# Performance work log

Hardware: AMD Instinct MI355X
Metric: run time of the kernel (lower is better)

## Reference

```python
import jax, jax.numpy as jnp
import numpy as np

DIM = 2048
HIDDEN = 2048
HEADS = 4
HD = HIDDEN // HEADS  # head_dim = 512
EPS = 1e-6
BATCH = 4
SEQ = 2048


def setup_inputs() -> dict:
    key = jax.random.key(0)
    k0, k1, k2, k3 = jax.random.split(key, 4)
    s = 0.02  # typical init scale; keeps exp() input gate well-behaved
    x = jax.random.normal(k0, (BATCH, SEQ, DIM), dtype=jnp.float32)
    W_in = (jax.random.normal(k1, (HIDDEN, DIM), dtype=jnp.float32) * s)
    W_gate = (jax.random.normal(k2, (4 * HIDDEN, HIDDEN), dtype=jnp.float32) * s)
    b_gate = jnp.zeros((4 * HIDDEN,), dtype=jnp.float32)
    rms_w = jnp.ones((HD,), dtype=jnp.float32)
    W_out = (jax.random.normal(k3, (DIM, HIDDEN), dtype=jnp.float32) * s)
    return {"x": x, "W_in": W_in, "W_gate": W_gate, "b_gate": b_gate,
            "rms_w": rms_w, "W_out": W_out}


def reference(x, W_in, W_gate, b_gate, rms_w, W_out):
    B, L, _ = x.shape
    # in_proj then gate_proj (the rearrange round-trip in torch is an identity
    # on the flat hidden dim, so gates come straight from x @ W_in.T)
    xp = x @ W_in.T                                    # (B, L, HIDDEN)
    gates = xp @ W_gate.T + b_gate                     # (B, L, 4*HIDDEN)
    # rearrange 'b l (h d) -> b h l d' with h=HEADS, d=4*HD
    gates = gates.reshape(B, L, HEADS, 4 * HD).transpose(0, 2, 1, 3)
    i_g, f_g, o_g, c_t = jnp.split(gates, 4, axis=-1)  # each (B, H, L, HD)
    i_g = jnp.exp(i_g)            # exponential input gate
    f_g = jax.nn.sigmoid(f_g)
    o_g = jax.nn.sigmoid(o_g)
    c_t = jnp.tanh(c_t)

    # time-major for the recurrent scan: (L, B, H, HD)
    tm = lambda a: jnp.moveaxis(a, 2, 0)

    def step(c, g):
        i, f, o, cd = g
        c = f * c + i * cd                                         # cell update
        c_norm = c * jax.lax.rsqrt(jnp.mean(c * c, axis=-1, keepdims=True) + EPS) * rms_w
        h = o * jnp.tanh(c_norm)
        return c, h

    c0 = jnp.zeros((B, HEADS, HD), dtype=x.dtype)
    _, hs = jax.lax.scan(step, c0, (tm(i_g), tm(f_g), tm(o_g), tm(c_t)))
    # (L, B, H, HD) -> (B, L, H*HD)
    h_out = jnp.moveaxis(hs, 0, 1).reshape(B, L, HIDDEN)
    return h_out @ W_out.T                             # (B, L, DIM)
```

## Files before the change

kernel.cpp:

```cpp
#include <hip/hip_runtime.h>
#include <hip/hip_bf16.h>
#include <stdint.h>

#define DIMN    2048
#define HIDDEN  2048
#define NHEADS  4
#define HDIM    512
#define BATCH   4
#define SEQ     2048
#define NTOK    (BATCH*SEQ)
#define G4      (4*HIDDEN)
#define EPSV    1e-6f
#define CHUNK   128
#define NCHUNK  (SEQ/CHUNK)

typedef short short8 __attribute__((ext_vector_type(8)));
typedef float floatx4 __attribute__((ext_vector_type(4)));

union BV8 { uint4 u; __hip_bfloat16 h[8]; unsigned short s[8]; };

__device__ __forceinline__ float fast_sigmoid(float x) {
    return 1.0f / (1.0f + __expf(-x));
}
__device__ __forceinline__ float fast_tanh(float x) {
    return 1.0f - 2.0f / (__expf(2.0f * x) + 1.0f);
}
__device__ __forceinline__ float b2f(unsigned short u) {
    union { unsigned int ui; float f; } v; v.ui = ((unsigned int)u) << 16; return v.f;
}

__device__ __forceinline__ void gld_lds16(const void* gp, void* lp) {
    __builtin_amdgcn_global_load_lds(
        (const __attribute__((address_space(1))) void*)gp,
        (__attribute__((address_space(3))) void*)lp, 16, 0, 0);
}

__global__ __launch_bounds__(256) void cast_f32_bf16(
    const float* __restrict__ in, __hip_bfloat16* __restrict__ out, int n8)
{
    int i = blockIdx.x * 256 + threadIdx.x;
    if (i >= n8) return;
    const float4* p = (const float4*)(in + (size_t)i * 8);
    float4 a = p[0], b = p[1];
    BV8 v;
    v.h[0] = __float2bfloat16(a.x); v.h[1] = __float2bfloat16(a.y);
    v.h[2] = __float2bfloat16(a.z); v.h[3] = __float2bfloat16(a.w);
    v.h[4] = __float2bfloat16(b.x); v.h[5] = __float2bfloat16(b.y);
    v.h[6] = __float2bfloat16(b.z); v.h[7] = __float2bfloat16(b.w);
    *(uint4*)(out + (size_t)i * 8) = v.u;
}

template <int EPILOGUE, int ASRC>
__global__ __launch_bounds__(512, 2) void gemm256(
    const __hip_bfloat16* __restrict__ A,
    const __hip_bfloat16* __restrict__ Bt,
    void* __restrict__ Cout,
    const float* __restrict__ bias,
    int M, int N, int K, int lda)
{
    __shared__ __align__(16) short sA[2][256 * 64];
    __shared__ __align__(16) short sB[2][256 * 64];

    const int tid  = threadIdx.x;
    const int wave = tid >> 6, lane = tid & 63;
    const int wm = wave >> 2, wn = wave & 3;
    const int quad = lane >> 4, lr = lane & 15;
    const int r8  = lane >> 3;
    const int gcs = ((lane & 7) ^ r8) * 8;
    const int rl7 = lr & 7;

    const int gx   = gridDim.x;
    const int nwg  = gx * gridDim.y;
    const int orig = blockIdx.y * gx + blockIdx.x;
    const int wg   = (orig & 7) * (nwg >> 3) + (orig >> 3);
    const int bm = wg / gx, bn = wg % gx;

    const short* Ag = (const short*)A + (size_t)(bm * 256) * lda;
    const short* Bg = (const short*)Bt + (size_t)(bn * 256) * K;

    floatx4 acc[8][4];
#pragma unroll
    for (int i = 0; i < 8; ++i)
#pragma unroll
        for (int j = 0; j < 4; ++j) acc[i][j] = (floatx4)0.0f;

    const int NT = K >> 6;

    auto stageA = [&](int kt, int qm) {
        const int kb = kt << 6;
        size_t acol;
        if (ASRC == 0) acol = (size_t)(kb + gcs);
        else           acol = (size_t)(((kb >> 9) << 11) + (kb & 511) + gcs);
        short* dst = &sA[kt & 1][0];
#pragma unroll
        for (int e = 0; e < 2; ++e) {
            const int base = qm * 128 + e * 64 + wave * 8;
            const int row  = base + r8;
            const int grow = ((row >> 6) & 1) * 128 + qm * 64 + (row & 63);
            gld_lds16(Ag + (size_t)grow * lda + acol, dst + base * 64);
        }
    };
    auto stageB = [&](int kt, int qn) {
        const int kb = kt << 6;
        short* dst = &sB[kt & 1][0];
#pragma unroll
        for (int e = 0; e < 2; ++e) {
            const int base = qn * 128 + e * 64 + wave * 8;
            const int row  = base + r8;
            const int grow = ((row >> 5) & 3) * 64 + qn * 32 + (row & 31);
            gld_lds16(Bg + (size_t)grow * K + kb + gcs, dst + base * 64);
        }
    };

    stageA(0, 0); stageB(0, 0); stageB(0, 1); stageA(0, 1);
    stageA(1, 0); stageB(1, 0); stageB(1, 1);
    asm volatile("s_waitcnt vmcnt(6)" ::: "memory");
    __builtin_amdgcn_s_barrier();

    short8 av[4][2], b0[2][2], b1[2][2];

    for (int t = 0; t < NT; ++t) {
        const short* lA = &sA[t & 1][0];
        const short* lB = &sB[t & 1][0];

#pragma unroll
        for (int kc = 0; kc < 2; ++kc) {
            const int co = (((kc * 4 + quad) ^ rl7) << 3);
#pragma unroll
            for (int m = 0; m < 4; ++m)
                av[m][kc] = *(const short8*)&lA[(wm * 64 + m * 16 + lr) * 64 + co];
#pragma unroll
            for (int j = 0; j < 2; ++j)
                b0[j][kc] = *(const short8*)&lB[(wn * 32 + j * 16 + lr) * 64 + co];
        }
        if (t + 1 < NT) stageA(t + 1, 1);
        __builtin_amdgcn_s_setprio(1);
#pragma unroll
        for (int m = 0; m < 4; ++m)
#pragma unroll
            for (int j = 0; j < 2; ++j)
#pragma unroll
                for (int kc = 0; kc < 2; ++kc)
                    acc[m][j] = __builtin_amdgcn_mfma_f32_16x16x32_bf16(
                        av[m][kc], b0[j][kc], acc[m][j], 0, 0, 0);
        __builtin_amdgcn_s_setprio(0);
        __builtin_amdgcn_s_barrier();

#pragma unroll
        for (int kc = 0; kc < 2; ++kc) {
            const int co = (((kc * 4 + quad) ^ rl7) << 3);
#pragma unroll
            for (int j = 0; j < 2; ++j)
                b1[j][kc] = *(const short8*)&lB[(128 + wn * 32 + j * 16 + lr) * 64 + co];
        }
        if (t + 2 < NT) stageA(t + 2, 0);
        __builtin_amdgcn_s_setprio(1);
#pragma unroll
        for (int m = 0; m < 4; ++m)
#pragma unroll
            for (int j = 0; j < 2; ++j)
#pragma unroll
                for (int kc = 0; kc < 2; ++kc)
                    acc[m][2 + j] = __builtin_amdgcn_mfma_f32_16x16x32_bf16(
                        av[m][kc], b1[j][kc], acc[m][2 + j], 0, 0, 0);
        __builtin_amdgcn_s_setprio(0);
        __builtin_amdgcn_s_barrier();

#pragma unroll
        for (int kc = 0; kc < 2; ++kc) {
            const int co = (((kc * 4 + quad) ^ rl7) << 3);
#pragma unroll
            for (int m = 0; m < 4; ++m)
                av[m][kc] = *(const short8*)&lA[(128 + wm * 64 + m * 16 + lr) * 64 + co];
        }
        if (t + 2 < NT) stageB(t + 2, 0);
        __builtin_amdgcn_s_setprio(1);
#pragma unroll
        for (int m = 0; m < 4; ++m)
#pragma unroll
            for (int j = 0; j < 2; ++j)
#pragma unroll
                for (int kc = 0; kc < 2; ++kc)
                    acc[4 + m][2 + j] = __builtin_amdgcn_mfma_f32_16x16x32_bf16(
                        av[m][kc], b1[j][kc], acc[4 + m][2 + j], 0, 0, 0);
        __builtin_amdgcn_s_setprio(0);
        __builtin_amdgcn_s_barrier();

        if (t + 2 < NT) stageB(t + 2, 1);
        __builtin_amdgcn_s_setprio(1);
#pragma unroll
        for (int m = 0; m < 4; ++m)
#pragma unroll
            for (int j = 0; j < 2; ++j)
#pragma unroll
                for (int kc = 0; kc < 2; ++kc)
                    acc[4 + m][j] = __builtin_amdgcn_mfma_f32_16x16x32_bf16(
                        av[m][kc], b0[j][kc], acc[4 + m][j], 0, 0, 0);
        __builtin_amdgcn_s_setprio(0);
        if (t < NT - 2)       asm volatile("s_waitcnt vmcnt(6)" ::: "memory");
        else if (t == NT - 2) asm volatile("s_waitcnt vmcnt(0)" ::: "memory");
        __builtin_amdgcn_s_barrier();
    }

    const int colbase = bn * 256 + wn * 64;
    const int rowbase = bm * 256 + wm * 128;

    if (EPILOGUE == 0) {
        __hip_bfloat16* O = (__hip_bfloat16*)Cout;
#pragma unroll
        for (int mt = 0; mt < 8; ++mt)
#pragma unroll
            for (int nt = 0; nt < 4; ++nt)
#pragma unroll
                for (int r = 0; r < 4; ++r) {
                    int row = rowbase + mt * 16 + quad * 4 + r;
                    int col = colbase + nt * 16 + lr;
                    O[(size_t)row * N + col] = __float2bfloat16(acc[mt][nt][r]);
                }
    } else if (EPILOGUE == 1) {
        __hip_bfloat16* O = (__hip_bfloat16*)Cout;
#pragma unroll
        for (int nt = 0; nt < 4; ++nt) {
            int col = colbase + nt * 16 + lr;
            int g = (col >> 9) & 3;
            float bv = bias[col];
#pragma unroll
            for (int mt = 0; mt < 8; ++mt)
#pragma unroll
                for (int r = 0; r < 4; ++r) {
                    int row = rowbase + mt * 16 + quad * 4 + r;
                    float v = acc[mt][nt][r] + bv;
                    if (g == 0)       v = __expf(v);
                    else if (g == 3)  v = fast_tanh(v);
                    else              v = fast_sigmoid(v);
                    O[(size_t)row * N + col] = __float2bfloat16(v);
                }
        }
    } else {
        float* O = (float*)Cout;
#pragma unroll
        for (int mt = 0; mt < 8; ++mt)
#pragma unroll
            for (int nt = 0; nt < 4; ++nt)
#pragma unroll
                for (int r = 0; r < 4; ++r) {
                    int row = rowbase + mt * 16 + quad * 4 + r;
                    int col = colbase + nt * 16 + lr;
                    O[(size_t)row * N + col] = acc[mt][nt][r];
                }
    }
}

struct G16 { unsigned short i[16], f[16], c[16]; };

__device__ __forceinline__ void load_g16(const unsigned short* __restrict__ g,
                                         int t0, G16& o)
{
#pragma unroll
    for (int j = 0; j < 16; ++j) {
        const unsigned short* gp = g + (size_t)(t0 + j) * G4;
        o.i[j] = gp[0]; o.f[j] = gp[512]; o.c[j] = gp[1536];
    }
}
__device__ __forceinline__ void comp_sum16(const G16& gg, float& c, float& P)
{
#pragma unroll
    for (int j = 0; j < 16; ++j) {
        float iv = b2f(gg.i[j]);
        float fv = b2f(gg.f[j]);
        float cd = b2f(gg.c[j]);
        c = fmaf(fv, c, iv * cd);
        P *= fv;
    }
}
__device__ __forceinline__ float comp_lds16(const G16& gg, float c,
                                            __hip_bfloat16* __restrict__ sc,
                                            int t0, int d)
{
#pragma unroll
    for (int j = 0; j < 16; ++j) {
        float iv = b2f(gg.i[j]);
        float fv = b2f(gg.f[j]);
        float cd = b2f(gg.c[j]);
        c = fmaf(fv, c, iv * cd);
        sc[(t0 + j) * HDIM + d] = __float2bfloat16(c);
    }
    return c;
}

__global__ __launch_bounds__(256) void scan_pass1(
    const __hip_bfloat16* __restrict__ gates,
    float* __restrict__ cLast, float* __restrict__ PLast)
{
    int blk = blockIdx.x;
    int dh = blk & 1;
    int j  = (blk >> 1) & 15;
    int bh = blk >> 5;
    int b = bh >> 2, h = bh & 3;
    int d = dh * 256 + threadIdx.x;
    int bhd = bh * 512 + d;

    const unsigned short* g = (const unsigned short*)gates
        + (size_t)(b * SEQ + j * CHUNK) * G4 + h * 2048 + d;

    float c = 0.0f, P = 1.0f;
    G16 A, B;
    load_g16(g, 0, A);
    for (int t0 = 0; t0 < CHUNK; t0 += 32) {
        load_g16(g, t0 + 16, B);
        comp_sum16(A, c, P);
        if (t0 + 32 < CHUNK) load_g16(g, t0 + 32, A);
        comp_sum16(B, c, P);
    }
    cLast[j * 8192 + bhd] = c;
    PLast[j * 8192 + bhd] = P;
}

__global__ __launch_bounds__(512) void scan_pass2_norm(
    const __hip_bfloat16* __restrict__ gates_c,
    const float* __restrict__ cLast, const float* __restrict__ PLast,
    __hip_bfloat16* __restrict__ gates,
    const float* __restrict__ rms_w)
{
    __shared__ __hip_bfloat16 sc[CHUNK * HDIM];

    int blk = blockIdx.x;
    int j  = blk & 15;
    int bh = blk >> 4;
    int b = bh >> 2, h = bh & 3;
    int d = threadIdx.x;
    int bhd = bh * 512 + d;

    float c = 0.0f;
    for (int k = 0; k < j; ++k)
        c = fmaf(PLast[k * 8192 + bhd], c, cLast[k * 8192 + bhd]);

    const unsigned short* g = (const unsigned short*)gates_c
        + (size_t)(b * SEQ + j * CHUNK) * G4 + h * 2048 + d;

    G16 A, B;
    load_g16(g, 0, A);
    for (int t0 = 0; t0 < CHUNK; t0 += 32) {
        load_g16(g, t0 + 16, B);
        c = comp_lds16(A, c, sc, t0, d);
        if (t0 + 32 < CHUNK) load_g16(g, t0 + 32, A);
        c = comp_lds16(B, c, sc, t0 + 16, d);
    }
    __syncthreads();

    const int wave = threadIdx.x >> 6, lane = threadIdx.x & 63;

    float4 w0 = *(const float4*)&rms_w[lane * 8];
    float4 w1 = *(const float4*)&rms_w[lane * 8 + 4];
    float w[8] = { w0.x, w0.y, w0.z, w0.w, w1.x, w1.y, w1.z, w1.w };

    for (int it = 0; it < 16; ++it) {
        int t = wave * 16 + it;
        size_t tok = (size_t)(b * SEQ + j * CHUNK + t);

        BV8 cv; cv.u = *(const uint4*)&sc[t * HDIM + lane * 8];
        float cf[8]; float s = 0.0f;
#pragma unroll
        for (int q = 0; q < 8; ++q) { cf[q] = b2f(cv.s[q]); s += cf[q] * cf[q]; }
#pragma unroll
        for (int off = 32; off > 0; off >>= 1) s += __shfl_xor(s, off, 64);
        float rs = rsqrtf(s * (1.0f / 512.0f) + EPSV);

        BV8 ov; ov.u = *(const uint4*)(gates + tok * G4 + h * 2048 + 1024 + lane * 8);
        BV8 hv;
#pragma unroll
        for (int q = 0; q < 8; ++q) {
            float o = b2f(ov.s[q]);
            hv.h[q] = __float2bfloat16(o * fast_tanh(cf[q] * rs * w[q]));
        }
        *(uint4*)(gates + tok * G4 + h * 2048 + lane * 8) = hv.u;
    }
}

extern "C" void kernel_launch(void* const* d_in, const int* in_sizes, int n_in,
                              void* d_out, int out_size, void* d_ws, size_t ws_size,
                              hipStream_t stream)
{
    const float* x      = (const float*)d_in[0];
    const float* W_in   = (const float*)d_in[1];
    const float* W_gate = (const float*)d_in[2];
    const float* b_gate = (const float*)d_in[3];
    const float* rms_w  = (const float*)d_in[4];
    const float* W_out  = (const float*)d_in[5];
    float* out = (float*)d_out;

    char* base = (char*)d_ws;
    __hip_bfloat16* wgb   = (__hip_bfloat16*)base;
    __hip_bfloat16* xpb   = (__hip_bfloat16*)(base + (((size_t)32) << 20));
    __hip_bfloat16* gates = (__hip_bfloat16*)(base + (((size_t)64) << 20));
    __hip_bfloat16* wib  = gates;
    __hip_bfloat16* xb   = (__hip_bfloat16*)(base + (((size_t)72) << 20));
    __hip_bfloat16* wob  = wgb;
    float* cLast = (float*)(base + (((size_t)8) << 20));
    float* PLast = (float*)(base + (((size_t)8) << 20) + (512 << 10));

    cast_f32_bf16<<<(HIDDEN * DIMN) / 8 / 256, 256, 0, stream>>>(W_in, wib, (HIDDEN * DIMN) / 8);
    cast_f32_bf16<<<(NTOK * DIMN) / 8 / 256, 256, 0, stream>>>(x, xb, (NTOK * DIMN) / 8);
    cast_f32_bf16<<<(G4 * HIDDEN) / 8 / 256, 256, 0, stream>>>(W_gate, wgb, (G4 * HIDDEN) / 8);

    {
        dim3 grid(HIDDEN / 256, NTOK / 256);
        gemm256<0, 0><<<grid, 512, 0, stream>>>(xb, wib, xpb, nullptr,
                                                NTOK, HIDDEN, DIMN, DIMN);
    }
    {
        dim3 grid(G4 / 256, NTOK / 256);
        gemm256<1, 0><<<grid, 512, 0, stream>>>(xpb, wgb, gates, b_gate,
                                                NTOK, G4, HIDDEN, HIDDEN);
    }
    cast_f32_bf16<<<(DIMN * HIDDEN) / 8 / 256, 256, 0, stream>>>(W_out, wob, (DIMN * HIDDEN) / 8);

    scan_pass1<<<BATCH * NHEADS * NCHUNK * 2, 256, 0, stream>>>(gates, cLast, PLast);
    scan_pass2_norm<<<BATCH * NHEADS * NCHUNK, 512, 0, stream>>>(gates, cLast, PLast,
                                                                 gates, rms_w);

    {
        dim3 grid(DIMN / 256, NTOK / 256);
        gemm256<2, 1><<<grid, 512, 0, stream>>>(gates, wob, out, nullptr,
                                                NTOK, DIMN, HIDDEN, G4);
    }
}
```

Baseline: 636.7 us.

## Rework GEMM to 4 waves with 128x128 per-wave tiles and simpler pipeline

The 256x256 GEMM moves from 8 waves (each computing 128x64) to 4 waves (each computing 128x128 with 64 accumulators), which raises register reuse of the A and B fragments. The staggered quarter-tile staging with partial vmcnt waits and s_setprio is replaced by one combined A+B stage per k-step, a full vmcnt(0) wait and a single barrier. This cuts LDS read traffic per MFMA and barrier count, but needs much higher register pressure (256 accumulator VGPRs), allows at most one block per CU, and loads the next tile less overlapped with compute.

```diff
diff --git a/kernel.cpp b/kernel.cpp
--- a/kernel.cpp
+++ b/kernel.cpp
@@ -51,7 +51,7 @@
 }
 
 template <int EPILOGUE, int ASRC>
-__global__ __launch_bounds__(512, 2) void gemm256(
+__global__ __launch_bounds__(256, 1) void gemm256(
     const __hip_bfloat16* __restrict__ A,
     const __hip_bfloat16* __restrict__ Bt,
     void* __restrict__ Cout,
@@ -63,7 +63,7 @@
 
     const int tid  = threadIdx.x;
     const int wave = tid >> 6, lane = tid & 63;
-    const int wm = wave >> 2, wn = wave & 3;
+    const int wm = wave >> 1, wn = wave & 1;
     const int quad = lane >> 4, lr = lane & 15;
     const int r8  = lane >> 3;
     const int gcs = ((lane & 7) ^ r8) * 8;
@@ -78,131 +78,78 @@
     const short* Ag = (const short*)A + (size_t)(bm * 256) * lda;
     const short* Bg = (const short*)Bt + (size_t)(bn * 256) * K;
 
-    floatx4 acc[8][4];
+    floatx4 acc[8][8];
 #pragma unroll
     for (int i = 0; i < 8; ++i)
 #pragma unroll
-        for (int j = 0; j < 4; ++j) acc[i][j] = (floatx4)0.0f;
+        for (int j = 0; j < 8; ++j) acc[i][j] = (floatx4)0.0f;
 
     const int NT = K >> 6;
 
-    auto stageA = [&](int kt, int qm) {
+    auto stageAB = [&](int kt) {
         const int kb = kt << 6;
         size_t acol;
         if (ASRC == 0) acol = (size_t)(kb + gcs);
         else           acol = (size_t)(((kb >> 9) << 11) + (kb & 511) + gcs);
-        short* dst = &sA[kt & 1][0];
-#pragma unroll
-        for (int e = 0; e < 2; ++e) {
-            const int base = qm * 128 + e * 64 + wave * 8;
-            const int row  = base + r8;
-            const int grow = ((row >> 6) & 1) * 128 + qm * 64 + (row & 63);
-            gld_lds16(Ag + (size_t)grow * lda + acol, dst + base * 64);
+        short* dA = &sA[kt & 1][0];
+        short* dB = &sB[kt & 1][0];
+#pragma unroll
+        for (int c = 0; c < 8; ++c) {
+            const int base = c * 32 + wave * 8;
+            const int grow = base + r8;
+            gld_lds16(Ag + (size_t)grow * lda + acol,   dA + base * 64);
+            gld_lds16(Bg + (size_t)grow * K + kb + gcs, dB + base * 64);
         }
     };
-    auto stageB = [&](int kt, int qn) {
-        const int kb = kt << 6;
-        short* dst = &sB[kt & 1][0];
-#pragma unroll
-        for (int e = 0; e < 2; ++e) {
-            const int base = qn * 128 + e * 64 + wave * 8;
-            const int row  = base + r8;
-            const int grow = ((row >> 5) & 3) * 64 + qn * 32 + (row & 31);
-            gld_lds16(Bg + (size_t)grow * K + kb + gcs, dst + base * 64);
-        }
-    };
-
-    stageA(0, 0); stageB(0, 0); stageB(0, 1); stageA(0, 1);
-    stageA(1, 0); stageB(1, 0); stageB(1, 1);
-    asm volatile("s_waitcnt vmcnt(6)" ::: "memory");
+
+    stageAB(0);
+    asm volatile("s_waitcnt vmcnt(0)" ::: "memory");
     __builtin_amdgcn_s_barrier();
 
-    short8 av[4][2], b0[2][2], b1[2][2];
+    short8 av[8], bv[8];
 
     for (int t = 0; t < NT; ++t) {
         const short* lA = &sA[t & 1][0];
         const short* lB = &sB[t & 1][0];
 
-#pragma unroll
-        for (int kc = 0; kc < 2; ++kc) {
-            const int co = (((kc * 4 + quad) ^ rl7) << 3);
-#pragma unroll
-            for (int m = 0; m < 4; ++m)
-                av[m][kc] = *(const short8*)&lA[(wm * 64 + m * 16 + lr) * 64 + co];
-#pragma unroll
-            for (int j = 0; j < 2; ++j)
-                b0[j][kc] = *(const short8*)&lB[(wn * 32 + j * 16 + lr) * 64 + co];
-        }
-        if (t + 1 < NT) stageA(t + 1, 1);
-        __builtin_amdgcn_s_setprio(1);
-#pragma unroll
-        for (int m = 0; m < 4; ++m)
-#pragma unroll
-            for (int j = 0; j < 2; ++j)
-#pragma unroll
-                for (int kc = 0; kc < 2; ++kc)
-                    acc[m][j] = __builtin_amdgcn_mfma_f32_16x16x32_bf16(
-                        av[m][kc], b0[j][kc], acc[m][j], 0, 0, 0);
-        __builtin_amdgcn_s_setprio(0);
+        {
+            const int co = ((quad ^ rl7) << 3);
+#pragma unroll
+            for (int mt = 0; mt < 8; ++mt)
+                av[mt] = *(const short8*)&lA[(wm * 128 + mt * 16 + lr) * 64 + co];
+#pragma unroll
+            for (int nt = 0; nt < 8; ++nt)
+                bv[nt] = *(const short8*)&lB[(wn * 128 + nt * 16 + lr) * 64 + co];
+        }
+        if (t + 1 < NT) stageAB(t + 1);
+#pragma unroll
+        for (int mt = 0; mt < 8; ++mt)
+#pragma unroll
+            for (int nt = 0; nt < 8; ++nt)
+                acc[mt][nt] = __builtin_amdgcn_mfma_f32_16x16x32_bf16(
+                    av[mt], bv[nt], acc[mt][nt], 0, 0, 0);
+
+        {
+            const int co = (((4 + quad) ^ rl7) << 3);
+#pragma unroll
+            for (int mt = 0; mt < 8; ++mt)
+                av[mt] = *(const short8*)&lA[(wm * 128 + mt * 16 + lr) * 64 + co];
+#pragma unroll
+            for (int nt = 0; nt < 8; ++nt)
+                bv[nt] = *(const short8*)&lB[(wn * 128 + nt * 16 + lr) * 64 + co];
+        }
+#pragma unroll
+        for (int mt = 0; mt < 8; ++mt)
+#pragma unroll
+            for (int nt = 0; nt < 8; ++nt)
+                acc[mt][nt] = __builtin_amdgcn_mfma_f32_16x16x32_bf16(
+                    av[mt], bv[nt], acc[mt][nt], 0, 0, 0);
+
+        if (t + 1 < NT) asm volatile("s_waitcnt vmcnt(0)" ::: "memory");
         __builtin_amdgcn_s_barrier();
-
-#pragma unroll
-        for (int kc = 0; kc < 2; ++kc) {
-            const int co = (((kc * 4 + quad) ^ rl7) << 3);
-#pragma unroll
-            for (int j = 0; j < 2; ++j)
-                b1[j][kc] = *(const short8*)&lB[(128 + wn * 32 + j * 16 + lr) * 64 + co];
-        }
-        if (t + 2 < NT) stageA(t + 2, 0);
-        __builtin_amdgcn_s_setprio(1);
-#pragma unroll
-        for (int m = 0; m < 4; ++m)
-#pragma unroll
-            for (int j = 0; j < 2; ++j)
-#pragma unroll
-                for (int kc = 0; kc < 2; ++kc)
-                    acc[m][2 + j] = __builtin_amdgcn_mfma_f32_16x16x32_bf16(
-                        av[m][kc], b1[j][kc], acc[m][2 + j], 0, 0, 0);
-        __builtin_amdgcn_s_setprio(0);
-        __builtin_amdgcn_s_barrier();
-
-#pragma unroll
-        for (int kc = 0; kc < 2; ++kc) {
-            const int co = (((kc * 4 + quad) ^ rl7) << 3);
-#pragma unroll
-            for (int m = 0; m < 4; ++m)
-                av[m][kc] = *(const short8*)&lA[(128 + wm * 64 + m * 16 + lr) * 64 + co];
-        }
-        if (t + 2 < NT) stageB(t + 2, 0);
-        __builtin_amdgcn_s_setprio(1);
-#pragma unroll
-        for (int m = 0; m < 4; ++m)
-#pragma unroll
-            for (int j = 0; j < 2; ++j)
-#pragma unroll
-                for (int kc = 0; kc < 2; ++kc)
-                    acc[4 + m][2 + j] = __builtin_amdgcn_mfma_f32_16x16x32_bf16(
-                        av[m][kc], b1[j][kc], acc[4 + m][2 + j], 0, 0, 0);
-        __builtin_amdgcn_s_setprio(0);
-        __builtin_amdgcn_s_barrier();
-
-        if (t + 2 < NT) stageB(t + 2, 1);
-        __builtin_amdgcn_s_setprio(1);
-#pragma unroll
-        for (int m = 0; m < 4; ++m)
-#pragma unroll
-            for (int j = 0; j < 2; ++j)
-#pragma unroll
-                for (int kc = 0; kc < 2; ++kc)
-                    acc[4 + m][j] = __builtin_amdgcn_mfma_f32_16x16x32_bf16(
-                        av[m][kc], b0[j][kc], acc[4 + m][j], 0, 0, 0);
-        __builtin_amdgcn_s_setprio(0);
-        if (t < NT - 2)       asm volatile("s_waitcnt vmcnt(6)" ::: "memory");
-        else if (t == NT - 2) asm volatile("s_waitcnt vmcnt(0)" ::: "memory");
-        __builtin_amdgcn_s_barrier();
-    }
-
-    const int colbase = bn * 256 + wn * 64;
+    }
+
+    const int colbase = bn * 256 + wn * 128;
     const int rowbase = bm * 256 + wm * 128;
 
     if (EPILOGUE == 0) {
@@ -210,7 +157,7 @@
 #pragma unroll
         for (int mt = 0; mt < 8; ++mt)
 #pragma unroll
-            for (int nt = 0; nt < 4; ++nt)
+            for (int nt = 0; nt < 8; ++nt)
 #pragma unroll
                 for (int r = 0; r < 4; ++r) {
                     int row = rowbase + mt * 16 + quad * 4 + r;
@@ -220,16 +167,16 @@
     } else if (EPILOGUE == 1) {
         __hip_bfloat16* O = (__hip_bfloat16*)Cout;
 #pragma unroll
-        for (int nt = 0; nt < 4; ++nt) {
+        for (int nt = 0; nt < 8; ++nt) {
             int col = colbase + nt * 16 + lr;
             int g = (col >> 9) & 3;
-            float bv = bias[col];
+            float bvs = bias[col];
 #pragma unroll
             for (int mt = 0; mt < 8; ++mt)
 #pragma unroll
                 for (int r = 0; r < 4; ++r) {
                     int row = rowbase + mt * 16 + quad * 4 + r;
-                    float v = acc[mt][nt][r] + bv;
+                    float v = acc[mt][nt][r] + bvs;
                     if (g == 0)       v = __expf(v);
                     else if (g == 3)  v = fast_tanh(v);
                     else              v = fast_sigmoid(v);
@@ -241,7 +188,7 @@
 #pragma unroll
         for (int mt = 0; mt < 8; ++mt)
 #pragma unroll
-            for (int nt = 0; nt < 4; ++nt)
+            for (int nt = 0; nt < 8; ++nt)
 #pragma unroll
                 for (int r = 0; r < 4; ++r) {
                     int row = rowbase + mt * 16 + quad * 4 + r;
@@ -405,12 +352,12 @@
 
     {
         dim3 grid(HIDDEN / 256, NTOK / 256);
-        gemm256<0, 0><<<grid, 512, 0, stream>>>(xb, wib, xpb, nullptr,
+        gemm256<0, 0><<<grid, 256, 0, stream>>>(xb, wib, xpb, nullptr,
                                                 NTOK, HIDDEN, DIMN, DIMN);
     }
     {
         dim3 grid(G4 / 256, NTOK / 256);
-        gemm256<1, 0><<<grid, 512, 0, stream>>>(xpb, wgb, gates, b_gate,
+        gemm256<1, 0><<<grid, 256, 0, stream>>>(xpb, wgb, gates, b_gate,
                                                 NTOK, G4, HIDDEN, HIDDEN);
     }
     cast_f32_bf16<<<(DIMN * HIDDEN) / 8 / 256, 256, 0, stream>>>(W_out, wob, (DIMN * HIDDEN) / 8);
@@ -421,7 +368,7 @@
 
     {
         dim3 grid(DIMN / 256, NTOK / 256);
-        gemm256<2, 1><<<grid, 512, 0, stream>>>(gates, wob, out, nullptr,
+        gemm256<2, 1><<<grid, 256, 0, stream>>>(gates, wob, out, nullptr,
                                                 NTOK, DIMN, HIDDEN, G4);
     }
 }
```

After: 750.2 us. 17.8% more time.
